# Kernel tuning notes

Hardware: AMD Instinct MI355X
Metric: run time of the kernel (lower is better)

## Reference

```python
import jax, jax.numpy as jnp
import numpy as np

NS_STEPS = 10
NS_A, NS_B, NS_C = 3.4445, -4.7750, 2.0315  # standard quintic Newton-Schulz coefficients
EPS = 1e-7

def orthogonalize(w):
    """Newton-Schulz iteration producing a (near-)orthogonal matrix from w."""
    din, dout = w.shape
    transpose = din > dout  # iterate on the wide orientation so X @ X.T is small
    x = w.T if transpose else w
    x = x / (jnp.linalg.norm(x) + EPS)  # spectral norm <= frobenius norm -> contraction

    def body(x, _):
        a = x @ x.T                      # (m, m) Gram matrix
        bmat = NS_B * a + NS_C * (a @ a)
        x = NS_A * x + bmat @ x
        return x, None

    x, _ = jax.lax.scan(body, x, None, length=NS_STEPS)
    return x.T if transpose else x


def setup_inputs() -> dict:
    key = jax.random.key(0)
    k1, k2, k3 = jax.random.split(key, 3)
    B, DIN, DOUT = 16384, 2048, 2048
    x = jax.random.normal(k1, (B, DIN), dtype=jnp.float32)
    w = jax.random.normal(k2, (DIN, DOUT), dtype=jnp.float32)
    b = jax.random.normal(k3, (DOUT,), dtype=jnp.float32) * 0.02
    return {"x": x, "w": w, "b": b}


def reference(x, w, b):
    w_orth = orthogonalize(w)
    return x @ w_orth + b
```

## Files before the change

kernel.cpp:

```cpp
#include <hip/hip_runtime.h>
#include <stdint.h>

typedef unsigned short u16;
typedef _Float16 half_t;
typedef __attribute__((ext_vector_type(4))) float f32x4;
typedef __attribute__((ext_vector_type(8))) _Float16 f16x8;

#define NS_A 3.4445f
#define NS_B -4.7750f
#define NS_C 2.0315f

#define SX      64.0f
#define INV_SX  (1.0f / 64.0f)
#define INV_SA  (1.0f / 4096.0f)

typedef const __attribute__((address_space(1))) void* as1_cvp;
typedef __attribute__((address_space(3))) void* as3_vp;
#define GLOAD_LDS16(gp, lp) \
    __builtin_amdgcn_global_load_lds((as1_cvp)(const void*)(gp), (as3_vp)(void*)(lp), 16, 0, 0)

#define BK 64

template <int MODE, bool SWZ, int BMt, int BNt>
__global__ __launch_bounds__(256, 3) void gemm_nt(
    const half_t* __restrict__ A, const half_t* __restrict__ B,
    const half_t* __restrict__ aux, const float* __restrict__ bias,
    void* __restrict__ outp, half_t* __restrict__ outpT,
    int M, int N, int K)
{
    constexpr int M_REP = BMt / 32;
    constexpr int N_REP = BNt / 32;

    __shared__ half_t As[2][BMt * BK];
    __shared__ half_t Bs[2][BNt * BK];
    const int tid  = threadIdx.x;
    const int wave = tid >> 6;
    const int lane = tid & 63;

    int bid = blockIdx.x;
    if (SWZ) {
        const int cpx = gridDim.x >> 3;
        bid = (bid & 7) * cpx + (bid >> 3);
    }
    const int nbx  = N / BNt;
    const int brow = (bid / nbx) * BMt;
    const int bcol = (bid % nbx) * BNt;
    const int wr = wave >> 1, wc = wave & 1;

    f32x4 acc[M_REP][N_REP] = {};

    const int r0  = tid >> 3;
    const int c8s = (((tid & 7) ^ ((tid >> 3) & 7))) * 8;

    const half_t* gA = A + (size_t)(brow + r0) * K + c8s;
    const half_t* gB = B + (size_t)(bcol + r0) * K + c8s;

    auto stage = [&](int buf, int kt) {
#pragma unroll
        for (int j = 0; j < BMt / 32; ++j)
            GLOAD_LDS16(gA + (size_t)(j * 32) * K + kt, &As[buf][(size_t)(j * 256 + wave * 64) * 8]);
#pragma unroll
        for (int j = 0; j < BNt / 32; ++j)
            GLOAD_LDS16(gB + (size_t)(j * 32) * K + kt, &Bs[buf][(size_t)(j * 256 + wave * 64) * 8]);
    };

    stage(0, 0);
    __syncthreads();

    const int nsteps = K / BK;
    for (int s = 0; s < nsteps; ++s) {
        const int cur = s & 1;
        if (s + 1 < nsteps) stage(cur ^ 1, (s + 1) * BK);

        f16x8 af[M_REP][2], bfr[N_REP][2];
#pragma unroll
        for (int m = 0; m < M_REP; ++m) {
            const int row = wr * (BMt / 2) + m * 16 + (lane & 15);
#pragma unroll
            for (int kk = 0; kk < 2; ++kk) {
                const int cc = (kk * 4 + (lane >> 4)) ^ (row & 7);
                af[m][kk] = *(const f16x8*)&As[cur][row * BK + cc * 8];
            }
        }
#pragma unroll
        for (int n = 0; n < N_REP; ++n) {
            const int row = wc * (BNt / 2) + n * 16 + (lane & 15);
#pragma unroll
            for (int kk = 0; kk < 2; ++kk) {
                const int cc = (kk * 4 + (lane >> 4)) ^ (row & 7);
                bfr[n][kk] = *(const f16x8*)&Bs[cur][row * BK + cc * 8];
            }
        }
#pragma unroll
        for (int kk = 0; kk < 2; ++kk)
#pragma unroll
            for (int m = 0; m < M_REP; ++m)
#pragma unroll
                for (int n = 0; n < N_REP; ++n)
                    acc[m][n] = __builtin_amdgcn_mfma_f32_16x16x32_f16(af[m][kk], bfr[n][kk], acc[m][n], 0, 0, 0);

        __syncthreads();
    }

#pragma unroll
    for (int m = 0; m < M_REP; ++m) {
#pragma unroll
        for (int n = 0; n < N_REP; ++n) {
            const int row0 = brow + wr * (BMt / 2) + m * 16 + (lane >> 4) * 4;
            const int col  = bcol + wc * (BNt / 2) + n * 16 + (lane & 15);
#pragma unroll
            for (int r = 0; r < 4; ++r) {
                const size_t idx = (size_t)(row0 + r) * N + col;
                const float v = acc[m][n][r];
                if (MODE == 0) {
                    ((half_t*)outp)[idx] = (half_t)v;
                } else if (MODE == 1) {
                    ((half_t*)outp)[idx] = (half_t)(NS_B * (float)aux[idx] + NS_C * v * INV_SA);
                } else if (MODE == 2) {
                    const half_t o = (half_t)(NS_A * (float)aux[idx] + v * INV_SA);
                    ((half_t*)outp)[idx] = o;
                    if (outpT) outpT[(size_t)col * M + row0 + r] = o;
                } else {
                    ((float*)outp)[idx] = v * INV_SX + bias[col];
                }
            }
        }
    }
}

__global__ __launch_bounds__(512, 2) void gemm_fin(
    const half_t* __restrict__ A, const half_t* __restrict__ B,
    const float* __restrict__ bias, float* __restrict__ out,
    int M, int N, int K)
{
    __shared__ half_t As[4][256 * 32];
    __shared__ half_t Bs[4][256 * 32];
    const int tid  = threadIdx.x;
    const int wid  = tid >> 6;
    const int lane = tid & 63;
    const int wm = wid >> 2;
    const int wn = wid & 3;

    int bid = blockIdx.x;
    const int cpx = gridDim.x >> 3;
    bid = (bid & 7) * cpx + (bid >> 3);
    const int nbx  = N >> 8;
    const int brow = (bid / nbx) << 8;
    const int bcol = (bid % nbx) << 8;

    f32x4 acc[8][4] = {};

    const half_t* gA = A + (size_t)(brow + (tid >> 2)) * K + (tid & 3) * 8;
    const half_t* gB = B + (size_t)(bcol + (tid >> 2)) * K + (tid & 3) * 8;

    int kt_next = 96;
    auto stage = [&](int slot, int kt) {
#pragma unroll
        for (int j = 0; j < 2; ++j)
            GLOAD_LDS16(gA + (size_t)(j * 128) * K + kt, &As[slot][(j * 512 + wid * 64) * 8]);
#pragma unroll
        for (int j = 0; j < 2; ++j)
            GLOAD_LDS16(gB + (size_t)(j * 128) * K + kt, &Bs[slot][(j * 512 + wid * 64) * 8]);
    };
    auto compute = [&](int slot) {
        f16x8 af[8], bf[4];
#pragma unroll
        for (int fr = 0; fr < 8; ++fr)
            af[fr] = *(const f16x8*)&As[slot][(wm * 128 + fr * 16 + (lane & 15)) * 32 + (lane >> 4) * 8];
#pragma unroll
        for (int fc = 0; fc < 4; ++fc)
            bf[fc] = *(const f16x8*)&Bs[slot][(wn * 64 + fc * 16 + (lane & 15)) * 32 + (lane >> 4) * 8];
#pragma unroll
        for (int fr = 0; fr < 8; ++fr)
#pragma unroll
            for (int fc = 0; fc < 4; ++fc)
                acc[fr][fc] = __builtin_amdgcn_mfma_f32_16x16x32_f16(af[fr], bf[fc], acc[fr][fc], 0, 0, 0);
    };

    stage(0, 0);
    stage(1, 32);
    stage(2, 64);

#define FIN_STEP(SLOT, DOSTAGE, VMN) \
    do { \
        if (DOSTAGE) { stage((SLOT + 3) & 3, kt_next); kt_next += 32; } \
        asm volatile("s_waitcnt vmcnt(" #VMN ")" ::: "memory"); \
        __builtin_amdgcn_s_barrier(); \
        compute(SLOT); \
        __builtin_amdgcn_s_barrier(); \
    } while (0)

    const int nouter = ((K >> 5) - 4) >> 2;
    for (int tt = 0; tt < nouter; ++tt) {
        FIN_STEP(0, true, 12);
        FIN_STEP(1, true, 12);
        FIN_STEP(2, true, 12);
        FIN_STEP(3, true, 12);
    }
    FIN_STEP(0, true, 12);
    FIN_STEP(1, false, 8);
    FIN_STEP(2, false, 4);
    FIN_STEP(3, false, 0);
#undef FIN_STEP

#pragma unroll
    for (int fr = 0; fr < 8; ++fr) {
#pragma unroll
        for (int fc = 0; fc < 4; ++fc) {
            const int row0 = brow + wm * 128 + fr * 16 + (lane >> 4) * 4;
            const int col  = bcol + wn * 64 + fc * 16 + (lane & 15);
            const float bv = bias[col];
#pragma unroll
            for (int r = 0; r < 4; ++r)
                out[(size_t)(row0 + r) * N + col] = acc[fr][fc][r] * INV_SX + bv;
        }
    }
}

__global__ __launch_bounds__(256) void k_sumsq(const float* __restrict__ w,
                                               float* __restrict__ part, int n) {
    __shared__ float s[256];
    const int per  = n / 1024;
    const int base = blockIdx.x * per;
    float acc = 0.f;
    for (int i = threadIdx.x; i < per; i += 256) {
        float v = w[base + i];
        acc += v * v;
    }
    s[threadIdx.x] = acc;
    __syncthreads();
    for (int k = 128; k > 0; k >>= 1) {
        if (threadIdx.x < k) s[threadIdx.x] += s[threadIdx.x + k];
        __syncthreads();
    }
    if (threadIdx.x == 0) part[blockIdx.x] = s[0];
}

__global__ __launch_bounds__(256) void k_scalefin(const float* __restrict__ part,
                                                  float* __restrict__ scale) {
    __shared__ float s[256];
    float acc = 0.f;
    for (int i = threadIdx.x; i < 1024; i += 256) acc += part[i];
    s[threadIdx.x] = acc;
    __syncthreads();
    for (int k = 128; k > 0; k >>= 1) {
        if (threadIdx.x < k) s[threadIdx.x] += s[threadIdx.x + k];
        __syncthreads();
    }
    if (threadIdx.x == 0) scale[0] = SX / (sqrtf(s[0]) + 1e-7f);
}

__global__ __launch_bounds__(256) void k_scale_f16(const float* __restrict__ w,
                                                   const float* __restrict__ scale,
                                                   half_t* __restrict__ o, int n) {
    const int i = (blockIdx.x * 256 + threadIdx.x) * 4;
    if (i < n) {
        const float sc = scale[0];
        float4 v = *(const float4*)(w + i);
        o[i + 0] = (half_t)(v.x * sc);
        o[i + 1] = (half_t)(v.y * sc);
        o[i + 2] = (half_t)(v.z * sc);
        o[i + 3] = (half_t)(v.w * sc);
    }
}

__global__ __launch_bounds__(256) void k_cast_f16(const float* __restrict__ w,
                                                  half_t* __restrict__ o, int n) {
    const int i = (blockIdx.x * 256 + threadIdx.x) * 4;
    if (i < n) {
        float4 v = *(const float4*)(w + i);
        o[i + 0] = (half_t)v.x;
        o[i + 1] = (half_t)v.y;
        o[i + 2] = (half_t)v.z;
        o[i + 3] = (half_t)v.w;
    }
}

__global__ __launch_bounds__(256) void k_transpose(const u16* __restrict__ in,
                                                   u16* __restrict__ out, int n) {
    __shared__ u16 tile[64][65];
    const int bx = blockIdx.x * 64, by = blockIdx.y * 64;
    const int tx = threadIdx.x & 63, ty = threadIdx.x >> 6;
    for (int i = ty; i < 64; i += 4) tile[i][tx] = in[(size_t)(by + i) * n + bx + tx];
    __syncthreads();
    for (int i = ty; i < 64; i += 4) out[(size_t)(bx + i) * n + by + tx] = tile[tx][i];
}

extern "C" void kernel_launch(void* const* d_in, const int* in_sizes, int n_in,
                              void* d_out, int out_size, void* d_ws, size_t ws_size,
                              hipStream_t stream) {
    const float* x = (const float*)d_in[0];
    const float* w = (const float*)d_in[1];
    const float* b = (const float*)d_in[2];
    float* out = (float*)d_out;

    const int D  = 2048;
    const int Bm = in_sizes[0] / D;
    const int WN = D * D;
    const int XN = Bm * D;

    const size_t matB = (size_t)WN * 2;
    const bool pingpong = ws_size >= 8192 + 6 * matB + (size_t)XN * 2;

    char* ws = (char*)d_ws;
    float* part  = (float*)ws;
    float* scale = part + 1024;
    half_t* xb0  = (half_t*)(ws + 8192);
    half_t* xb1  = xb0 + WN;
    half_t* xbTa = xb1 + WN;
    half_t* xbTb = pingpong ? (xbTa + WN) : xbTa;
    half_t* amat = xbTb + WN;
    half_t* bmat = amat + WN;
    half_t* xinb = bmat + WN;

    k_sumsq<<<1024, 256, 0, stream>>>(w, part, WN);
    k_scalefin<<<1, 256, 0, stream>>>(part, scale);
    k_scale_f16<<<WN / 4 / 256, 256, 0, stream>>>(w, scale, xb0, WN);

    k_cast_f16<<<XN / 4 / 256, 256, 0, stream>>>(x, xinb, XN);

    const dim3 tgrid(D / 64, D / 64);
    k_transpose<<<tgrid, 256, 0, stream>>>((const u16*)xb0, (u16*)xbTa, D);

    const int ns_grid = (D / 64) * (D / 128);

    half_t* cur = xb0;
    half_t* nxt = xb1;
    half_t* Tr  = xbTa;
    half_t* Tw  = xbTb;
    for (int it = 0; it < 10; ++it) {
        gemm_nt<0, true, 64, 128><<<ns_grid, 256, 0, stream>>>(cur, cur, nullptr, nullptr, amat, nullptr, D, D, D);
        gemm_nt<1, true, 64, 128><<<ns_grid, 256, 0, stream>>>(amat, amat, amat, nullptr, bmat, nullptr, D, D, D);
        if (pingpong) {
            gemm_nt<2, true, 64, 128><<<ns_grid, 256, 0, stream>>>(bmat, Tr, cur, nullptr, nxt, Tw, D, D, D);
            half_t* tt = Tr; Tr = Tw; Tw = tt;
        } else {
            gemm_nt<2, true, 64, 128><<<ns_grid, 256, 0, stream>>>(bmat, Tr, cur, nullptr, nxt, nullptr, D, D, D);
            k_transpose<<<tgrid, 256, 0, stream>>>((const u16*)nxt, (u16*)Tr, D);
        }
        half_t* t = cur; cur = nxt; nxt = t;
    }

    const int fin_grid = (Bm / 256) * (D / 256);
    gemm_fin<<<fin_grid, 512, 0, stream>>>(xinb, Tr, b, out, Bm, D, D);
}
```

Measured before the change: 1.117 ms.

## Triple-buffer NS GEMM pipeline, swizzle final GEMM LDS, and split its fragment loads

The Newton-Schulz GEMM moves from double to triple buffering. It issues the LDS fragment reads before the next global-to-LDS prefetch, waits on explicit vmcnt counts, and raises wave priority around the MFMA block. The final large GEMM gets an XOR swizzle on its LDS layout to cut bank conflicts, and its A-fragment reads are split in two halves interleaved with MFMAs to lower register pressure. The extra LDS buffer lowers the occupancy hint from 3 to 2 blocks per CU, which may reduce latency hiding.

```diff
diff --git a/kernel.cpp b/kernel.cpp
--- a/kernel.cpp
+++ b/kernel.cpp
@@ -19,95 +19,114 @@
 #define GLOAD_LDS16(gp, lp) \
     __builtin_amdgcn_global_load_lds((as1_cvp)(const void*)(gp), (as3_vp)(void*)(lp), 16, 0, 0)
 
-#define BK 64
-
-template <int MODE, bool SWZ, int BMt, int BNt>
-__global__ __launch_bounds__(256, 3) void gemm_nt(
+template <int N> __device__ __forceinline__ void vmwait() {
+    if constexpr (N == 0)      asm volatile("s_waitcnt vmcnt(0)" ::: "memory");
+    else if constexpr (N == 4) asm volatile("s_waitcnt vmcnt(4)" ::: "memory");
+    else if constexpr (N == 6) asm volatile("s_waitcnt vmcnt(6)" ::: "memory");
+    else if constexpr (N == 8) asm volatile("s_waitcnt vmcnt(8)" ::: "memory");
+    else static_assert(N == 0, "unsupported vmcnt");
+}
+
+template <int MODE>
+__global__ __launch_bounds__(256, 2) void gemm_ns(
     const half_t* __restrict__ A, const half_t* __restrict__ B,
-    const half_t* __restrict__ aux, const float* __restrict__ bias,
+    const half_t* __restrict__ aux,
     void* __restrict__ outp, half_t* __restrict__ outpT,
     int M, int N, int K)
 {
-    constexpr int M_REP = BMt / 32;
-    constexpr int N_REP = BNt / 32;
-
-    __shared__ half_t As[2][BMt * BK];
-    __shared__ half_t Bs[2][BNt * BK];
+    __shared__ half_t As[3][64 * 64];
+    __shared__ half_t Bs[3][128 * 64];
     const int tid  = threadIdx.x;
-    const int wave = tid >> 6;
+    const int wid  = tid >> 6;
     const int lane = tid & 63;
+    const int wr = wid >> 1, wc = wid & 1;
 
     int bid = blockIdx.x;
-    if (SWZ) {
-        const int cpx = gridDim.x >> 3;
-        bid = (bid & 7) * cpx + (bid >> 3);
-    }
-    const int nbx  = N / BNt;
-    const int brow = (bid / nbx) * BMt;
-    const int bcol = (bid % nbx) * BNt;
-    const int wr = wave >> 1, wc = wave & 1;
-
-    f32x4 acc[M_REP][N_REP] = {};
-
-    const int r0  = tid >> 3;
-    const int c8s = (((tid & 7) ^ ((tid >> 3) & 7))) * 8;
-
-    const half_t* gA = A + (size_t)(brow + r0) * K + c8s;
-    const half_t* gB = B + (size_t)(bcol + r0) * K + c8s;
-
-    auto stage = [&](int buf, int kt) {
-#pragma unroll
-        for (int j = 0; j < BMt / 32; ++j)
-            GLOAD_LDS16(gA + (size_t)(j * 32) * K + kt, &As[buf][(size_t)(j * 256 + wave * 64) * 8]);
-#pragma unroll
-        for (int j = 0; j < BNt / 32; ++j)
-            GLOAD_LDS16(gB + (size_t)(j * 32) * K + kt, &Bs[buf][(size_t)(j * 256 + wave * 64) * 8]);
-    };
-
-    stage(0, 0);
-    __syncthreads();
-
-    const int nsteps = K / BK;
-    for (int s = 0; s < nsteps; ++s) {
-        const int cur = s & 1;
-        if (s + 1 < nsteps) stage(cur ^ 1, (s + 1) * BK);
-
-        f16x8 af[M_REP][2], bfr[N_REP][2];
-#pragma unroll
-        for (int m = 0; m < M_REP; ++m) {
-            const int row = wr * (BMt / 2) + m * 16 + (lane & 15);
+    const int cpx = gridDim.x >> 3;
+    bid = (bid & 7) * cpx + (bid >> 3);
+    const int nbx  = N / 128;
+    const int brow = (bid / nbx) * 64;
+    const int bcol = (bid % nbx) * 128;
+
+    f32x4 acc[2][4] = {};
+
+    const int r0   = tid >> 3;
+    const int csrc = ((tid & 7) ^ ((tid >> 3) & 7)) * 8;
+    const half_t* gA = A + (size_t)(brow + r0) * K + csrc;
+    const half_t* gB = B + (size_t)(bcol + r0) * K + csrc;
+
+    auto stage = [&](int slot, int kt) {
+#pragma unroll
+        for (int j = 0; j < 2; ++j)
+            GLOAD_LDS16(gA + (size_t)(j * 32) * K + kt, &As[slot][(j * 256 + wid * 64) * 8]);
+#pragma unroll
+        for (int j = 0; j < 4; ++j)
+            GLOAD_LDS16(gB + (size_t)(j * 32) * K + kt, &Bs[slot][(j * 256 + wid * 64) * 8]);
+    };
+
+    f16x8 af[2][2], bf[4][2];
+    auto reads = [&](int slot) {
+#pragma unroll
+        for (int m = 0; m < 2; ++m) {
+            const int row = wr * 32 + m * 16 + (lane & 15);
 #pragma unroll
             for (int kk = 0; kk < 2; ++kk) {
                 const int cc = (kk * 4 + (lane >> 4)) ^ (row & 7);
-                af[m][kk] = *(const f16x8*)&As[cur][row * BK + cc * 8];
+                af[m][kk] = *(const f16x8*)&As[slot][row * 64 + cc * 8];
             }
         }
 #pragma unroll
-        for (int n = 0; n < N_REP; ++n) {
-            const int row = wc * (BNt / 2) + n * 16 + (lane & 15);
+        for (int n = 0; n < 4; ++n) {
+            const int row = wc * 64 + n * 16 + (lane & 15);
 #pragma unroll
             for (int kk = 0; kk < 2; ++kk) {
                 const int cc = (kk * 4 + (lane >> 4)) ^ (row & 7);
-                bfr[n][kk] = *(const f16x8*)&Bs[cur][row * BK + cc * 8];
+                bf[n][kk] = *(const f16x8*)&Bs[slot][row * 64 + cc * 8];
             }
         }
+    };
+    auto mfma = [&]() {
+        __builtin_amdgcn_s_setprio(1);
 #pragma unroll
         for (int kk = 0; kk < 2; ++kk)
 #pragma unroll
-            for (int m = 0; m < M_REP; ++m)
-#pragma unroll
-                for (int n = 0; n < N_REP; ++n)
-                    acc[m][n] = __builtin_amdgcn_mfma_f32_16x16x32_f16(af[m][kk], bfr[n][kk], acc[m][n], 0, 0, 0);
-
-        __syncthreads();
-    }
-
-#pragma unroll
-    for (int m = 0; m < M_REP; ++m) {
-#pragma unroll
-        for (int n = 0; n < N_REP; ++n) {
-            const int row0 = brow + wr * (BMt / 2) + m * 16 + (lane >> 4) * 4;
-            const int col  = bcol + wc * (BNt / 2) + n * 16 + (lane & 15);
+            for (int m = 0; m < 2; ++m)
+#pragma unroll
+                for (int n = 0; n < 4; ++n)
+                    acc[m][n] = __builtin_amdgcn_mfma_f32_16x16x32_f16(af[m][kk], bf[n][kk], acc[m][n], 0, 0, 0);
+        __builtin_amdgcn_s_setprio(0);
+    };
+
+    const int nsteps = K / 64;
+    stage(0, 0);
+    stage(1, 64);
+    vmwait<6>();
+    __builtin_amdgcn_s_barrier();
+
+    int s = 0;
+    for (; s < nsteps - 2; ++s) {
+        reads(s % 3);
+        stage((s + 2) % 3, (s + 2) * 64);
+        vmwait<6>();
+        __builtin_amdgcn_s_barrier();
+        mfma();
+        __builtin_amdgcn_s_barrier();
+    }
+    reads(s % 3);
+    vmwait<0>();
+    __builtin_amdgcn_s_barrier();
+    mfma();
+    __builtin_amdgcn_s_barrier();
+    ++s;
+    reads(s % 3);
+    mfma();
+
+#pragma unroll
+    for (int m = 0; m < 2; ++m) {
+#pragma unroll
+        for (int n = 0; n < 4; ++n) {
+            const int row0 = brow + wr * 32 + m * 16 + (lane >> 4) * 4;
+            const int col  = bcol + wc * 64 + n * 16 + (lane & 15);
 #pragma unroll
             for (int r = 0; r < 4; ++r) {
                 const size_t idx = (size_t)(row0 + r) * N + col;
@@ -116,12 +135,10 @@
                     ((half_t*)outp)[idx] = (half_t)v;
                 } else if (MODE == 1) {
                     ((half_t*)outp)[idx] = (half_t)(NS_B * (float)aux[idx] + NS_C * v * INV_SA);
-                } else if (MODE == 2) {
+                } else {
                     const half_t o = (half_t)(NS_A * (float)aux[idx] + v * INV_SA);
                     ((half_t*)outp)[idx] = o;
                     if (outpT) outpT[(size_t)col * M + row0 + r] = o;
-                } else {
-                    ((float*)outp)[idx] = v * INV_SX + bias[col];
                 }
             }
         }
@@ -150,10 +167,11 @@
 
     f32x4 acc[8][4] = {};
 
-    const half_t* gA = A + (size_t)(brow + (tid >> 2)) * K + (tid & 3) * 8;
-    const half_t* gB = B + (size_t)(bcol + (tid >> 2)) * K + (tid & 3) * 8;
-
-    int kt_next = 96;
+    const int r0   = tid >> 2;
+    const int csrc = ((tid & 3) ^ ((tid >> 3) & 3)) * 8;
+    const half_t* gA = A + (size_t)(brow + r0) * K + csrc;
+    const half_t* gB = B + (size_t)(bcol + r0) * K + csrc;
+
     auto stage = [&](int slot, int kt) {
 #pragma unroll
         for (int j = 0; j < 2; ++j)
@@ -162,46 +180,70 @@
         for (int j = 0; j < 2; ++j)
             GLOAD_LDS16(gB + (size_t)(j * 128) * K + kt, &Bs[slot][(j * 512 + wid * 64) * 8]);
     };
-    auto compute = [&](int slot) {
-        f16x8 af[8], bf[4];
-#pragma unroll
-        for (int fr = 0; fr < 8; ++fr)
-            af[fr] = *(const f16x8*)&As[slot][(wm * 128 + fr * 16 + (lane & 15)) * 32 + (lane >> 4) * 8];
-#pragma unroll
-        for (int fc = 0; fc < 4; ++fc)
-            bf[fc] = *(const f16x8*)&Bs[slot][(wn * 64 + fc * 16 + (lane & 15)) * 32 + (lane >> 4) * 8];
-#pragma unroll
-        for (int fr = 0; fr < 8; ++fr)
+
+    f16x8 bf[4], af[4];
+    auto reads_pre = [&](int slot) {
+#pragma unroll
+        for (int fc = 0; fc < 4; ++fc) {
+            const int row = wn * 64 + fc * 16 + (lane & 15);
+            bf[fc] = *(const f16x8*)&Bs[slot][row * 32 + (((lane >> 4) ^ ((row >> 1) & 3)) * 8)];
+        }
+#pragma unroll
+        for (int fr = 0; fr < 4; ++fr) {
+            const int row = wm * 128 + fr * 16 + (lane & 15);
+            af[fr] = *(const f16x8*)&As[slot][row * 32 + (((lane >> 4) ^ ((row >> 1) & 3)) * 8)];
+        }
+    };
+    auto mfma_all = [&](int slot) {
+        __builtin_amdgcn_s_setprio(1);
+#pragma unroll
+        for (int fr = 0; fr < 4; ++fr)
 #pragma unroll
             for (int fc = 0; fc < 4; ++fc)
                 acc[fr][fc] = __builtin_amdgcn_mfma_f32_16x16x32_f16(af[fr], bf[fc], acc[fr][fc], 0, 0, 0);
-    };
-
+#pragma unroll
+        for (int fr = 0; fr < 4; ++fr) {
+            const int row = wm * 128 + (fr + 4) * 16 + (lane & 15);
+            af[fr] = *(const f16x8*)&As[slot][row * 32 + (((lane >> 4) ^ ((row >> 1) & 3)) * 8)];
+        }
+#pragma unroll
+        for (int fr = 0; fr < 4; ++fr)
+#pragma unroll
+            for (int fc = 0; fc < 4; ++fc)
+                acc[fr + 4][fc] = __builtin_amdgcn_mfma_f32_16x16x32_f16(af[fr], bf[fc], acc[fr + 4][fc], 0, 0, 0);
+        __builtin_amdgcn_s_setprio(0);
+    };
+
+    const int nsteps = K >> 5;
     stage(0, 0);
     stage(1, 32);
     stage(2, 64);
-
-#define FIN_STEP(SLOT, DOSTAGE, VMN) \
-    do { \
-        if (DOSTAGE) { stage((SLOT + 3) & 3, kt_next); kt_next += 32; } \
-        asm volatile("s_waitcnt vmcnt(" #VMN ")" ::: "memory"); \
-        __builtin_amdgcn_s_barrier(); \
-        compute(SLOT); \
-        __builtin_amdgcn_s_barrier(); \
-    } while (0)
-
-    const int nouter = ((K >> 5) - 4) >> 2;
-    for (int tt = 0; tt < nouter; ++tt) {
-        FIN_STEP(0, true, 12);
-        FIN_STEP(1, true, 12);
-        FIN_STEP(2, true, 12);
-        FIN_STEP(3, true, 12);
-    }
-    FIN_STEP(0, true, 12);
-    FIN_STEP(1, false, 8);
-    FIN_STEP(2, false, 4);
-    FIN_STEP(3, false, 0);
-#undef FIN_STEP
+    vmwait<8>();
+    __builtin_amdgcn_s_barrier();
+
+    int s = 0;
+    for (; s < nsteps - 3; ++s) {
+        reads_pre(s & 3);
+        stage((s + 3) & 3, (s + 3) * 32);
+        vmwait<8>();
+        __builtin_amdgcn_s_barrier();
+        mfma_all(s & 3);
+        __builtin_amdgcn_s_barrier();
+    }
+    reads_pre(s & 3);
+    vmwait<4>();
+    __builtin_amdgcn_s_barrier();
+    mfma_all(s & 3);
+    __builtin_amdgcn_s_barrier();
+    ++s;
+    reads_pre(s & 3);
+    vmwait<0>();
+    __builtin_amdgcn_s_barrier();
+    mfma_all(s & 3);
+    __builtin_amdgcn_s_barrier();
+    ++s;
+    reads_pre(s & 3);
+    mfma_all(s & 3);
 
 #pragma unroll
     for (int fr = 0; fr < 8; ++fr) {
@@ -329,13 +371,13 @@
     half_t* Tr  = xbTa;
     half_t* Tw  = xbTb;
     for (int it = 0; it < 10; ++it) {
-        gemm_nt<0, true, 64, 128><<<ns_grid, 256, 0, stream>>>(cur, cur, nullptr, nullptr, amat, nullptr, D, D, D);
-        gemm_nt<1, true, 64, 128><<<ns_grid, 256, 0, stream>>>(amat, amat, amat, nullptr, bmat, nullptr, D, D, D);
+        gemm_ns<0><<<ns_grid, 256, 0, stream>>>(cur, cur, nullptr, amat, nullptr, D, D, D);
+        gemm_ns<1><<<ns_grid, 256, 0, stream>>>(amat, amat, amat, bmat, nullptr, D, D, D);
         if (pingpong) {
-            gemm_nt<2, true, 64, 128><<<ns_grid, 256, 0, stream>>>(bmat, Tr, cur, nullptr, nxt, Tw, D, D, D);
+            gemm_ns<2><<<ns_grid, 256, 0, stream>>>(bmat, Tr, cur, nxt, Tw, D, D, D);
             half_t* tt = Tr; Tr = Tw; Tw = tt;
         } else {
-            gemm_nt<2, true, 64, 128><<<ns_grid, 256, 0, stream>>>(bmat, Tr, cur, nullptr, nxt, nullptr, D, D, D);
+            gemm_ns<2><<<ns_grid, 256, 0, stream>>>(bmat, Tr, cur, nxt, nullptr, D, D, D);
             k_transpose<<<tgrid, 256, 0, stream>>>((const u16*)nxt, (u16*)Tr, D);
         }
         half_t* t = cur; cur = nxt; nxt = t;
```

Measured after the change: 982.1 us. 12.1% less time.
